# Optimization experiments

Hardware: AMD Instinct MI355X
Metric: run time of the kernel (lower is better)

The kernel has to match this reference:

```python
import jax, jax.numpy as jnp
import numpy as np

HEAD, DIM, R = 8, 256, 3
RA = (2 * R + 1) ** 2  # 49


def conv2d(x, w, b=None, pad=0, groups=1):
    y = jax.lax.conv_general_dilated(x, w, (1, 1), [(pad, pad), (pad, pad)],
                                     dimension_numbers=('NCHW', 'OIHW', 'NCHW'),
                                     feature_group_count=groups)
    return y if b is None else y + b[None, :, None, None]


def grid_sample(img, grid, mode, padding='zeros'):
    # img [B,C,H,W]; grid [B,Hg,Wg,2] with (x,y) in [-1,1]; align_corners=False.
    B, C, H, W = img.shape
    Hg, Wg = grid.shape[1], grid.shape[2]
    gx = ((grid[..., 0] + 1.0) * W - 1.0) / 2.0
    gy = ((grid[..., 1] + 1.0) * H - 1.0) / 2.0
    if padding == 'border':
        gx = jnp.clip(gx, 0.0, W - 1.0)
        gy = jnp.clip(gy, 0.0, H - 1.0)
    gx = gx.reshape(B, -1)
    gy = gy.reshape(B, -1)

    def gather(iy, ix):
        iyc = jnp.clip(iy, 0, H - 1)
        ixc = jnp.clip(ix, 0, W - 1)
        return jax.vmap(lambda im, a, b: im[:, a, b])(img, iyc, ixc)  # [B,C,N]

    def mask(iy, ix):
        if padding == 'border':
            return jnp.ones(iy.shape, img.dtype)
        return ((ix >= 0) & (ix < W) & (iy >= 0) & (iy < H)).astype(img.dtype)

    if mode == 'nearest':
        ix = jnp.round(gx).astype(jnp.int32)
        iy = jnp.round(gy).astype(jnp.int32)
        out = gather(iy, ix) * mask(iy, ix)[:, None, :]
    else:  # bilinear
        x0f = jnp.floor(gx); y0f = jnp.floor(gy)
        wx = gx - x0f; wy = gy - y0f
        x0 = x0f.astype(jnp.int32); y0 = y0f.astype(jnp.int32)
        out = jnp.zeros((B, C, gx.shape[1]), img.dtype)
        for dx, dy, w in ((0, 0, (1 - wx) * (1 - wy)), (1, 0, wx * (1 - wy)),
                          (0, 1, (1 - wx) * wy), (1, 1, wx * wy)):
            ix = x0 + dx; iy = y0 + dy
            out = out + gather(iy, ix) * (w * mask(iy, ix))[:, None, :]
    return out.reshape(B, C, Hg, Wg)


def mlp2(x, W1, b1, W2, b2):
    return jax.nn.relu(x @ W1.T + b1) @ W2.T + b2


def setup_inputs() -> dict:
    key = jax.random.key(0)
    ks = jax.random.split(key, 32)
    B, H, W, Q = 1, 64, 64, 4096
    f32 = jnp.float32
    rn = lambda k, shp, s=0.02: jax.random.normal(k, shp, f32) * s
    return {
        'inp': jax.random.normal(ks[0], (B, 3, H, W), f32),
        'coord': jax.random.uniform(ks[1], (B, Q, 2), f32, -1.0, 1.0),
        'cell': jnp.full((B, Q, 2), 2.0 / (2 * H), f32),
        'W_enc': rn(ks[2], (64, 3, 3, 3)), 'b_enc': jnp.zeros((64,), f32),
        'W_ch': rn(ks[3], (256, 64, 3, 3)), 'b_ch': jnp.zeros((256,), f32),
        'W_q': rn(ks[4], (256, 256, 3, 3)), 'b_q': jnp.zeros((256,), f32),
        'W_k': rn(ks[5], (256, 256, 3, 3)), 'b_k': jnp.zeros((256,), f32),
        'W_v': rn(ks[6], (256, 256, 3, 3)), 'b_v': jnp.zeros((256,), f32),
        'W_off1': rn(ks[7], (256, 32, 5, 5)), 'b_off1': jnp.zeros((256,), f32),
        'ln_g': jnp.ones((256,), f32), 'ln_b': jnp.zeros((256,), f32),
        'W_off2': rn(ks[8], (98, 256, 1, 1)),
        'Wc1': rn(ks[9], (256, 98)), 'bc1': jnp.zeros((256,), f32),
        'Wc2': rn(ks[10], (49, 256)), 'bc2': jnp.zeros((49,), f32),
        'Wi1': rn(ks[11], (256, 12546)), 'bi1': jnp.zeros((256,), f32),
        'Wi2': rn(ks[12], (3, 256)), 'bi2': jnp.zeros((3,), f32),
        'scale': 2,
    }


def reference(inp, coord, cell, W_enc, b_enc, W_ch, b_ch, W_q, b_q, W_k, b_k,
              W_v, b_v, W_off1, b_off1, ln_g, ln_b, W_off2, Wc1, bc1, Wc2, bc2,
              Wi1, bi1, Wi2, bi2, scale):
    B, _, H, W = inp.shape
    Q = coord.shape[1]
    # gen_feat: encoder stub (conv+relu) -> conv_ch -> q/k/v convs
    feat = conv2d(jax.nn.relu(conv2d(inp, W_enc, b_enc, pad=1)), W_ch, b_ch, pad=1)
    fq = conv2d(feat, W_q, b_q, pad=1)
    fk = conv2d(feat, W_k, b_k, pad=1)
    fv = conv2d(feat, W_v, b_v, pad=1)
    # offset branch: grouped 5x5 conv -> channelwise LN -> GELU -> 1x1 conv (no bias)
    o = conv2d(feat, W_off1, b_off1, pad=2, groups=8)
    oc = o.transpose(0, 2, 3, 1)
    mu = oc.mean(-1, keepdims=True)
    var = ((oc - mu) ** 2).mean(-1, keepdims=True)
    oc = (oc - mu) / jnp.sqrt(var + 1e-5) * ln_g + ln_b
    offsets = conv2d(jax.nn.gelu(oc.transpose(0, 3, 1, 2), approximate=False), W_off2, None, pad=0)  # [B,98,H,W]
    # LR coordinate grid (y,x) at pixel centers in [-1,1]
    ys = -1.0 + 1.0 / H + (2.0 / H) * jnp.arange(H, dtype=inp.dtype)
    xs = -1.0 + 1.0 / W + (2.0 / W) * jnp.arange(W, dtype=inp.dtype)
    coord_lr = jnp.broadcast_to(jnp.stack(jnp.meshgrid(ys, xs, indexing='ij'), 0)[None], (B, 2, H, W))
    sc = coord[:, :, None, :]          # [B,Q,1,2] (y,x)
    g = sc[..., ::-1]                  # (x,y) for grid_sample
    sck = grid_sample(coord_lr, g, 'nearest').transpose(0, 2, 3, 1)  # [B,Q,1,2]
    off = grid_sample(offsets, g, 'nearest').transpose(0, 2, 3, 1).reshape(B, Q, RA, 2)
    off = jnp.tanh(off) * jnp.array([1.0 / (H - 1.0), 1.0 / (W - 1.0)], inp.dtype) * 2.0
    d = jnp.linspace(-R, R, 2 * R + 1).astype(inp.dtype)
    delta = jnp.stack(jnp.meshgrid(d * (2.0 / H), d * (2.0 / W), indexing='ij'), -1).reshape(1, 1, RA, 2)
    sck = sck + delta + off            # [B,Q,49,2] sampling locs (y,x)
    q = grid_sample(fq, g, 'bilinear').transpose(0, 2, 3, 1).reshape(B, Q, HEAD, DIM // HEAD)
    k = grid_sample(fk, sck[..., ::-1], 'nearest').transpose(0, 2, 3, 1).reshape(B, Q, RA, HEAD, DIM // HEAD)
    v = grid_sample(fv, sck[..., ::-1], 'nearest').transpose(0, 2, 3, 1).reshape(B, Q, RA, HEAD, DIM // HEAD)
    attn_val = jnp.einsum('bqhd,bqkhd->bqkh', q, k) / np.sqrt(DIM // HEAD)  # [B,Q,49,8]
    rel = (sc - sck) * jnp.array([H, W], inp.dtype)  # [B,Q,49,2]
    wcoord = mlp2(rel.reshape(B * Q, RA * 2), Wc1, bc1, Wc2, bc2).reshape(B, Q, RA, 1)
    attn = jax.nn.softmax(wcoord + attn_val, axis=2)  # softmax over 49 samples
    feat_in = (v * attn[..., None]).reshape(B, Q, RA * DIM)
    rel_cell = cell * jnp.array([H, W], inp.dtype)
    feat_in = jnp.concatenate([feat_in, rel_cell], -1)  # [B,Q,12546]
    pred = mlp2(feat_in.reshape(B * Q, -1), Wi1, bi1, Wi2, bi2).reshape(B, Q, 3)
    skip = grid_sample(inp, g, 'bilinear', 'border')[:, :, :, 0].transpose(0, 2, 1)
    return pred + skip
```

## Files before the change

### kernel.cpp

```cpp
#include <hip/hip_runtime.h>
#include <hip/hip_bf16.h>


typedef unsigned short u16;
typedef unsigned int u32;
using frag_ab = __attribute__((ext_vector_type(8))) short;
using frag_cd = __attribute__((ext_vector_type(4))) float;

#define HW 4096
#define NQ 4096
#define KBIG 12576
#define SPLITK 16
#define KCHUNK 800
#define KQ 2304
#define QSPLIT 3
#define QCHUNK 768
#define NBLK_QKV (64 * 6 * QSPLIT)
#define NBLK_OFF1 (64 * 8)

static __device__ __forceinline__ u16 f2b(float f) {
  union { __hip_bfloat16 h; u16 u; } c; c.h = __float2bfloat16(f); return c.u;
}
static __device__ __forceinline__ float b2f(u16 v) {
  return __uint_as_float((u32)v << 16);
}
static __device__ __forceinline__ u32 pk2(float a, float b) {
  union { __hip_bfloat162 h; u32 u; } c;
  c.h = __float22bfloat162_rn(float2{a, b});
  return c.u;
}
static __device__ __forceinline__ void glds16(const u16* g, u16* l) {
  __builtin_amdgcn_global_load_lds(
      (const __attribute__((address_space(1))) u32*)(g),
      (__attribute__((address_space(3))) u32*)(l), 16, 0, 0);
}

#define BM 64
#define BN 64
#define BK 32
#define LDSS 40

__global__ __launch_bounds__(256)
void gemm_bt(const u16* __restrict__ A, const u16* __restrict__ Bt,
             void* __restrict__ Cv, const float* __restrict__ bias,
             int N, int K, int ldc, int flags,
             long sA, long sB, long sC, int sBias)
{
  __shared__ u16 As[BM * LDSS];
  __shared__ u16 Bs[BN * LDSS];
  const int z = blockIdx.z;
  A  += (long)z * sA;
  Bt += (long)z * sB;
  const float* bz = bias ? bias + (long)z * sBias : nullptr;

  const int tid  = threadIdx.x;
  const int m0   = blockIdx.x * BM;
  const int n0   = blockIdx.y * BN;
  const int wave = tid >> 6, lane = tid & 63;
  const int mw = (wave & 1) * 32, nw = (wave >> 1) * 32;
  const int lr = lane & 15, lk = lane >> 4;
  const int srow = tid >> 2, scol = (tid & 3) * 8;

  frag_cd acc[2][2] = {};
  const u16* aptr = A + (size_t)(m0 + srow) * K + scol;
  const bool bok  = (n0 + srow) < N;
  const u16* bptr = Bt + (size_t)(n0 + srow) * K + scol;

  uint4 av = *(const uint4*)(aptr);
  uint4 bv = bok ? *(const uint4*)(bptr) : uint4{0u, 0u, 0u, 0u};

  for (int k0 = 0; k0 < K; k0 += BK) {
    *(uint4*)&As[srow * LDSS + scol] = av;
    *(uint4*)&Bs[srow * LDSS + scol] = bv;
    __syncthreads();
    if (k0 + BK < K) {
      av = *(const uint4*)(aptr + k0 + BK);
      bv = bok ? *(const uint4*)(bptr + k0 + BK) : uint4{0u, 0u, 0u, 0u};
    }
    frag_ab af0 = *(const frag_ab*)&As[(mw      + lr) * LDSS + lk * 8];
    frag_ab af1 = *(const frag_ab*)&As[(mw + 16 + lr) * LDSS + lk * 8];
    frag_ab bf0 = *(const frag_ab*)&Bs[(nw      + lr) * LDSS + lk * 8];
    frag_ab bf1 = *(const frag_ab*)&Bs[(nw + 16 + lr) * LDSS + lk * 8];
    acc[0][0] = __builtin_amdgcn_mfma_f32_16x16x32_bf16(af0, bf0, acc[0][0], 0, 0, 0);
    acc[0][1] = __builtin_amdgcn_mfma_f32_16x16x32_bf16(af0, bf1, acc[0][1], 0, 0, 0);
    acc[1][0] = __builtin_amdgcn_mfma_f32_16x16x32_bf16(af1, bf0, acc[1][0], 0, 0, 0);
    acc[1][1] = __builtin_amdgcn_mfma_f32_16x16x32_bf16(af1, bf1, acc[1][1], 0, 0, 0);
    __syncthreads();
  }

  const bool relu = flags & 1;
  const bool obf  = flags & 2;
  #pragma unroll
  for (int i = 0; i < 2; i++)
    #pragma unroll
    for (int j = 0; j < 2; j++) {
      int col = n0 + nw + j * 16 + lr;
      if (col >= N) continue;
      float badd = bz ? bz[col] : 0.f;
      #pragma unroll
      for (int r = 0; r < 4; r++) {
        int row = m0 + mw + i * 16 + lk * 4 + r;
        float v = acc[i][j][r] + badd;
        if (relu) v = fmaxf(v, 0.f);
        size_t idx = (size_t)z * sC + (size_t)row * ldc + col;
        if (obf) ((u16*)Cv)[idx] = f2b(v);
        else     ((float*)Cv)[idx] = v;
      }
    }
}

template<int W3, int SH, int PAD>
__global__ __launch_bounds__(256)
void gemm_conv(const u16* __restrict__ feat, const u16* __restrict__ Bt,
               void* __restrict__ Cv, const float* __restrict__ bias,
               int N, int K, int ldc, int flags, int FC, int cbStride,
               long sB, long sC, int sBias)
{
  __shared__ u16 As[BM * LDSS];
  __shared__ u16 Bs[BN * LDSS];
  const int z = blockIdx.z;
  Bt += (long)z * sB;
  const float* bz = bias ? bias + (long)z * sBias : nullptr;
  const int cb = z * cbStride;

  const int tid  = threadIdx.x;
  const int m0   = blockIdx.x * BM;
  const int n0   = blockIdx.y * BN;
  const int wave = tid >> 6, lane = tid & 63;
  const int mw = (wave & 1) * 32, nw = (wave >> 1) * 32;
  const int lr = lane & 15, lk = lane >> 4;
  const int srow = tid >> 2, scol = (tid & 3) * 8;
  const int p = m0 + srow, y = p >> 6, x = p & 63;

  frag_cd acc[2][2] = {};
  const bool bok  = (n0 + srow) < N;
  const u16* bptr = Bt + (size_t)(n0 + srow) * K + scol;

  auto stageA = [&](int k0) -> uint4 {
    int k = k0 + scol;
    int s = k >> SH;
    int c = k & ((1 << SH) - 1);
    int dy = s / W3, dx = s - dy * W3;
    int yy = y + dy - PAD, xx = x + dx - PAD;
    if (((unsigned)yy < 64u) && ((unsigned)xx < 64u))
      return *(const uint4*)&feat[(size_t)(yy * 64 + xx) * FC + cb + c];
    return uint4{0u, 0u, 0u, 0u};
  };

  uint4 av = stageA(0);
  uint4 bv = bok ? *(const uint4*)(bptr) : uint4{0u, 0u, 0u, 0u};

  for (int k0 = 0; k0 < K; k0 += BK) {
    *(uint4*)&As[srow * LDSS + scol] = av;
    *(uint4*)&Bs[srow * LDSS + scol] = bv;
    __syncthreads();
    if (k0 + BK < K) {
      av = stageA(k0 + BK);
      bv = bok ? *(const uint4*)(bptr + k0 + BK) : uint4{0u, 0u, 0u, 0u};
    }
    frag_ab af0 = *(const frag_ab*)&As[(mw      + lr) * LDSS + lk * 8];
    frag_ab af1 = *(const frag_ab*)&As[(mw + 16 + lr) * LDSS + lk * 8];
    frag_ab bf0 = *(const frag_ab*)&Bs[(nw      + lr) * LDSS + lk * 8];
    frag_ab bf1 = *(const frag_ab*)&Bs[(nw + 16 + lr) * LDSS + lk * 8];
    acc[0][0] = __builtin_amdgcn_mfma_f32_16x16x32_bf16(af0, bf0, acc[0][0], 0, 0, 0);
    acc[0][1] = __builtin_amdgcn_mfma_f32_16x16x32_bf16(af0, bf1, acc[0][1], 0, 0, 0);
    acc[1][0] = __builtin_amdgcn_mfma_f32_16x16x32_bf16(af1, bf0, acc[1][0], 0, 0, 0);
    acc[1][1] = __builtin_amdgcn_mfma_f32_16x16x32_bf16(af1, bf1, acc[1][1], 0, 0, 0);
    __syncthreads();
  }

  const bool relu = flags & 1;
  const bool obf  = flags & 2;
  #pragma unroll
  for (int i = 0; i < 2; i++)
    #pragma unroll
    for (int j = 0; j < 2; j++) {
      int col = n0 + nw + j * 16 + lr;
      if (col >= N) continue;
      float badd = bz ? bz[col] : 0.f;
      #pragma unroll
      for (int r = 0; r < 4; r++) {
        int row = m0 + mw + i * 16 + lk * 4 + r;
        float v = acc[i][j][r] + badd;
        if (relu) v = fmaxf(v, 0.f);
        size_t idx = (size_t)z * sC + (size_t)row * ldc + col;
        if (obf) ((u16*)Cv)[idx] = f2b(v);
        else     ((float*)Cv)[idx] = v;
      }
    }
}

__global__ __launch_bounds__(256)
void gemm_feat(const u16* __restrict__ feat, const u16* __restrict__ Btqkv,
               u16* __restrict__ Pq, const u16* __restrict__ Btoff1,
               float* __restrict__ obuf, const float* __restrict__ b_off1)
{
  __shared__ u16 smem[6656];
  const int bid = blockIdx.x;
  const int tid = threadIdx.x;
  const int wave = tid >> 6, lane = tid & 63;
  const int lr = lane & 15, lk = lane >> 4;

  if (bid < NBLK_QKV) {
    u16* As = smem;
    u16* Bs = smem + 64 * 40;
    const int mz  = bid & 63;
    const int rest = bid >> 6;
    const int ny  = rest % 6;
    const int z   = rest / 6;
    const int m0  = mz * 64;
    const int n0  = ny * 128;
    const int kbeg = z * QCHUNK;
    const int kend = kbeg + QCHUNK;
    const int nw = wave * 32;
    const int arow = tid >> 2, acol = (tid & 3) * 8;
    const int p = m0 + arow, y = p >> 6, x = p & 63;

    frag_cd acc[4][2] = {};
    const u16* bbase = Btqkv + (size_t)(n0 + (tid >> 2)) * KQ + (tid & 3) * 8 + kbeg;
    u16* bdst = &Bs[(size_t)tid * 8];

    auto stageA = [&](int k0) -> uint4 {
      int k = k0 + acol;
      int s = k >> 8, c = k & 255;
      int dy = s / 3, dx = s - dy * 3;
      int yy = y + dy - 1, xx = x + dx - 1;
      if (((unsigned)yy < 64u) && ((unsigned)xx < 64u))
        return *(const uint4*)&feat[(size_t)(yy * 64 + xx) * 256 + c];
      return uint4{0u, 0u, 0u, 0u};
    };

    uint4 av = stageA(kbeg);

    for (int k0 = kbeg; k0 < kend; k0 += BK) {
      glds16(bbase + (k0 - kbeg), bdst);
      glds16(bbase + (k0 - kbeg) + (size_t)64 * KQ, bdst + 2048);
      *(uint4*)&As[arow * LDSS + acol] = av;
      __syncthreads();
      if (k0 + BK < kend) av = stageA(k0 + BK);
      frag_ab af[4];
      #pragma unroll
      for (int i = 0; i < 4; i++)
        af[i] = *(const frag_ab*)&As[(i * 16 + lr) * LDSS + lk * 8];
      #pragma unroll
      for (int j = 0; j < 2; j++) {
        frag_ab bf = *(const frag_ab*)&Bs[(nw + j * 16 + lr) * 32 + lk * 8];
        #pragma unroll
        for (int i = 0; i < 4; i++)
          acc[i][j] = __builtin_amdgcn_mfma_f32_16x16x32_bf16(af[i], bf, acc[i][j], 0, 0, 0);
      }
      __syncthreads();
    }

    #pragma unroll
    for (int i = 0; i < 4; i++)
      #pragma unroll
      for (int j = 0; j < 2; j++) {
        int col = n0 + nw + j * 16 + lr;
        #pragma unroll
        for (int r = 0; r < 4; r++) {
          int row = m0 + i * 16 + lk * 4 + r;
          Pq[(size_t)z * (NQ * 768) + (size_t)row * 768 + col] = f2b(acc[i][j][r]);
        }
      }
  } else {
    u16* As = smem;
    u16* Bs = smem + 64 * 40;
    const int t  = bid - NBLK_QKV;
    const int m0 = (t & 63) * 64;
    const int g  = t >> 6;
    const int cb = g * 32;
    const u16* Bt = Btoff1 + (size_t)g * 32 * 800;
    const float* bz = b_off1 + g * 32;
    const int mw = (wave & 1) * 32, nw = (wave >> 1) * 32;
    const int srow = tid >> 2, scol = (tid & 3) * 8;
    const int p = m0 + srow, y = p >> 6, x = p & 63;

    frag_cd acc[2][2] = {};
    const bool bok  = srow < 32;
    const u16* bptr = Bt + (size_t)srow * 800 + scol;

    auto stageA = [&](int k0) -> uint4 {
      int k = k0 + scol;
      int s = k >> 5;
      int c = k & 31;
      int dy = s / 5, dx = s - dy * 5;
      int yy = y + dy - 2, xx = x + dx - 2;
      if (((unsigned)yy < 64u) && ((unsigned)xx < 64u))
        return *(const uint4*)&feat[(size_t)(yy * 64 + xx) * 256 + cb + c];
      return uint4{0u, 0u, 0u, 0u};
    };

    uint4 av = stageA(0);
    uint4 bv = bok ? *(const uint4*)(bptr) : uint4{0u, 0u, 0u, 0u};

    for (int k0 = 0; k0 < 800; k0 += BK) {
      *(uint4*)&As[srow * LDSS + scol] = av;
      *(uint4*)&Bs[srow * LDSS + scol] = bv;
      __syncthreads();
      if (k0 + BK < 800) {
        av = stageA(k0 + BK);
        bv = bok ? *(const uint4*)(bptr + k0 + BK) : uint4{0u, 0u, 0u, 0u};
      }
      frag_ab af0 = *(const frag_ab*)&As[(mw      + lr) * LDSS + lk * 8];
      frag_ab af1 = *(const frag_ab*)&As[(mw + 16 + lr) * LDSS + lk * 8];
      frag_ab bf0 = *(const frag_ab*)&Bs[(nw      + lr) * LDSS + lk * 8];
      frag_ab bf1 = *(const frag_ab*)&Bs[(nw + 16 + lr) * LDSS + lk * 8];
      acc[0][0] = __builtin_amdgcn_mfma_f32_16x16x32_bf16(af0, bf0, acc[0][0], 0, 0, 0);
      acc[0][1] = __builtin_amdgcn_mfma_f32_16x16x32_bf16(af0, bf1, acc[0][1], 0, 0, 0);
      acc[1][0] = __builtin_amdgcn_mfma_f32_16x16x32_bf16(af1, bf0, acc[1][0], 0, 0, 0);
      acc[1][1] = __builtin_amdgcn_mfma_f32_16x16x32_bf16(af1, bf1, acc[1][1], 0, 0, 0);
      __syncthreads();
    }

    #pragma unroll
    for (int i = 0; i < 2; i++)
      #pragma unroll
      for (int j = 0; j < 2; j++) {
        int col = nw + j * 16 + lr;
        if (col >= 32) continue;
        float badd = bz[col];
        #pragma unroll
        for (int r = 0; r < 4; r++) {
          int row = m0 + mw + i * 16 + lk * 4 + r;
          obuf[(size_t)row * 256 + g * 32 + col] = acc[i][j][r] + badd;
        }
      }
  }
}

__global__ __launch_bounds__(256)
void reduce_qkv(const u16* __restrict__ P, const float* __restrict__ bias,
                u16* __restrict__ outb, float* __restrict__ outV)
{
  int i8 = blockIdx.x * 256 + threadIdx.x;
  if (i8 >= NQ * 96) return;
  size_t i = (size_t)i8 * 8;
  int row = (int)(i / 768);
  int c = (int)(i % 768);
  float v[8];
  #pragma unroll
  for (int t = 0; t < 8; t++) v[t] = bias[c + t];
  for (int z = 0; z < QSPLIT; z++) {
    uint4 a = *(const uint4*)&P[(size_t)z * (NQ * 768) + i];
    u32 aw[4] = {a.x, a.y, a.z, a.w};
    #pragma unroll
    for (int t = 0; t < 4; t++) {
      v[2 * t]     += __uint_as_float(aw[t] << 16);
      v[2 * t + 1] += __uint_as_float(aw[t] & 0xffff0000u);
    }
  }
  uint4 ob = {pk2(v[0], v[1]), pk2(v[2], v[3]), pk2(v[4], v[5]), pk2(v[6], v[7])};
  *(uint4*)&outb[i] = ob;
  if (c >= 512) {
    float* dst = outV + (size_t)row * 256 + (c - 512);
    *(float4*)dst       = float4{v[0], v[1], v[2], v[3]};
    *(float4*)(dst + 4) = float4{v[4], v[5], v[6], v[7]};
  }
}

__global__ __launch_bounds__(512, 4)
void gemm_big(const u16* __restrict__ Bt, const float* __restrict__ fqkvV,
              const float* __restrict__ attnval, const int* __restrict__ vidx,
              const float* __restrict__ cell, u16* __restrict__ P)
{
  __shared__ u16 As[128 * LDSS];
  __shared__ u16 Bs[256 * 32];
  __shared__ int   s_vidx[5 * 128];
  __shared__ float s_attn[5 * 128 * 8];
  const int tid  = threadIdx.x;
  const int m0   = blockIdx.x * 128;
  const int z    = blockIdx.y;
  const int kbeg = z * KCHUNK;
  const int kend = min(KBIG, kbeg + KCHUNK);
  const int jbeg = kbeg >> 8;
  const int jcnt = ((kend - 1) >> 8) - jbeg + 1;
  const int wave = tid >> 6, lane = tid & 63;
  const int mw = (wave & 1) * 64, nwv = (wave >> 1) * 64;
  const int lr = lane & 15, lk = lane >> 4;
  const int arow = tid >> 2, acol = (tid & 3) * 8;
  const int q = m0 + arow;

  for (int t = tid; t < 128 * jcnt; t += 512) {
    int r = t & 127, jj = t >> 7;
    int j = jbeg + jj;
    s_vidx[t] = (j < 49) ? vidx[(m0 + r) * 49 + j] : -1;
  }
  for (int t = tid; t < 128 * 8 * jcnt; t += 512) {
    int h = t & 7, rr = (t >> 3) & 127, jj = t >> 10;
    int j = jbeg + jj;
    s_attn[t] = (j < 49) ? attnval[((size_t)((m0 + rr) * 49 + j)) * 8 + h] : 0.f;
  }
  __syncthreads();

  auto loadA = [&](int k0, float4& f0, float4& f1, float& w) {
    const int k = k0 + acol;
    const int j = k >> 8, c = k & 255;
    f0 = float4{0.f, 0.f, 0.f, 0.f};
    f1 = float4{0.f, 0.f, 0.f, 0.f};
    w = 0.f;
    if (j < 49) {
      const int jj = j - jbeg;
      int id = s_vidx[jj * 128 + arow];
      if (id >= 0) {
        w = s_attn[(jj * 128 + arow) * 8 + (c >> 5)];
        const float* src = fqkvV + (size_t)id * 256 + c;
        f0 = *(const float4*)src;
        f1 = *(const float4*)(src + 4);
      }
    } else if (c == 0) {
      f0.x = cell[q * 2]; f0.y = cell[q * 2 + 1];
      w = 64.f;
    }
  };

  frag_cd acc[4][4] = {};
  float4 f0c, f1c; float wc_;
  loadA(kbeg, f0c, f1c, wc_);
  const u16* bbase = Bt + (size_t)(tid >> 2) * KBIG + (tid & 3) * 8 + kbeg;
  u16* bdst = &Bs[(size_t)tid * 8];

  for (int k0 = kbeg; k0 < kend; k0 += BK) {
    glds16(bbase + (k0 - kbeg), bdst);
    glds16(bbase + (k0 - kbeg) + (size_t)128 * KBIG, bdst + 4096);
    {
      uint4 av;
      av.x = pk2(f0c.x * wc_, f0c.y * wc_);
      av.y = pk2(f0c.z * wc_, f0c.w * wc_);
      av.z = pk2(f1c.x * wc_, f1c.y * wc_);
      av.w = pk2(f1c.z * wc_, f1c.w * wc_);
      *(uint4*)&As[arow * LDSS + acol] = av;
    }
    __syncthreads();
    if (k0 + BK < kend) loadA(k0 + BK, f0c, f1c, wc_);
    frag_ab af[4];
    #pragma unroll
    for (int i = 0; i < 4; i++)
      af[i] = *(const frag_ab*)&As[(mw + i * 16 + lr) * LDSS + lk * 8];
    #pragma unroll
    for (int j = 0; j < 4; j++) {
      frag_ab bf = *(const frag_ab*)&Bs[(nwv + j * 16 + lr) * 32 + lk * 8];
      #pragma unroll
      for (int i = 0; i < 4; i++)
        acc[i][j] = __builtin_amdgcn_mfma_f32_16x16x32_bf16(af[i], bf, acc[i][j], 0, 0, 0);
    }
    __syncthreads();
  }

  #pragma unroll
  for (int i = 0; i < 4; i++)
    #pragma unroll
    for (int j = 0; j < 4; j++) {
      int col = nwv + j * 16 + lr;
      #pragma unroll
      for (int r = 0; r < 4; r++) {
        int row = m0 + mw + i * 16 + lk * 4 + r;
        P[(size_t)z * (NQ * 256) + (size_t)row * 256 + col] = f2b(acc[i][j][r]);
      }
    }
}

__global__ __launch_bounds__(256)
void reduce_final(const u16* __restrict__ Pb, const float* __restrict__ bi1,
                  const float* __restrict__ Wi2, const float* __restrict__ bi2,
                  const float* __restrict__ skipb, float* __restrict__ out)
{
  const int q = blockIdx.x, c = threadIdx.x;
  float s = 0.f;
  #pragma unroll
  for (int z = 0; z < SPLITK; z++)
    s += b2f(Pb[(size_t)z * (NQ * 256) + (size_t)q * 256 + c]);
  s += bi1[c];
  s = fmaxf(s, 0.f);

  __shared__ float part[3][4];
  float p0 = s * Wi2[c], p1 = s * Wi2[256 + c], p2 = s * Wi2[512 + c];
  #pragma unroll
  for (int off = 32; off; off >>= 1) {
    p0 += __shfl_xor(p0, off);
    p1 += __shfl_xor(p1, off);
    p2 += __shfl_xor(p2, off);
  }
  if ((c & 63) == 0) {
    int w = c >> 6;
    part[0][w] = p0; part[1][w] = p1; part[2][w] = p2;
  }
  __syncthreads();
  if (c < 3)
    out[q * 3 + c] = bi2[c] + skipb[q * 3 + c]
                   + part[c][0] + part[c][1] + part[c][2] + part[c][3];
}

__global__ __launch_bounds__(512)
void softmax_k(const float* __restrict__ wc, float* __restrict__ attnval)
{
  const int q = blockIdx.x;
  const int tid = threadIdx.x;
  const int hh = tid >> 6, l = tid & 63;
  float v = (l < 49) ? wc[(size_t)q * 49 + l] + attnval[((size_t)q * 49 + l) * 8 + hh]
                     : -1e30f;
  float m = v;
  #pragma unroll
  for (int off = 32; off; off >>= 1) m = fmaxf(m, __shfl_xor(m, off));
  float e = (l < 49) ? expf(v - m) : 0.f;
  float s = e;
  #pragma unroll
  for (int off = 32; off; off >>= 1) s += __shfl_xor(s, off);
  if (l < 49) attnval[((size_t)q * 49 + l) * 8 + hh] = e / s;
}

static __device__ __forceinline__
void packconv(const float* __restrict__ W, u16* __restrict__ Bt,
              int Cin, int K2, int idx)
{
  int o  = idx / (Cin * K2);
  int r  = idx - o * (Cin * K2);
  int ci = r / K2;
  int s  = r - ci * K2;
  Bt[(size_t)o * (Cin * K2) + s * Cin + ci] = f2b(W[idx]);
}
static __device__ __forceinline__
void packcast(const float* __restrict__ W, u16* __restrict__ Bt,
              int Kin, int Kout, int idx)
{
  int n = idx / Kout, k = idx - n * Kout;
  Bt[idx] = f2b(k < Kin ? W[(size_t)n * Kin + k] : 0.f);
}

#define SZ_CH   147456
#define SZ_QKV  589824
#define SZ_OFF1 204800
#define SZ_OFF2 25088
#define SZ_C1   32768
#define SZ_C2   12544
#define SZ_WI1  3219456
#define SZ_PACK (SZ_CH + 3*SZ_QKV + SZ_OFF1 + SZ_OFF2 + SZ_C1 + SZ_C2 + 768 + SZ_WI1)

__global__ void pack_all(const float* W_ch, const float* W_q, const float* W_k,
                         const float* W_v, const float* W_off1, const float* W_off2,
                         const float* Wc1, const float* Wc2, const float* Wi1,
                         const float* b_q, const float* b_k, const float* b_v,
                         u16* Btch, u16* Btqkv, u16* Btoff1, u16* Btoff2,
                         u16* Btc1, u16* Btc2, u16* Wi1p, float* bqkv)
{
  int i = blockIdx.x * 256 + threadIdx.x;
  if (i < SZ_CH) { packconv(W_ch, Btch, 64, 9, i); return; }
  i -= SZ_CH;
  if (i < SZ_QKV) { packconv(W_q, Btqkv, 256, 9, i); return; }
  i -= SZ_QKV;
  if (i < SZ_QKV) { packconv(W_k, Btqkv + (size_t)256 * 2304, 256, 9, i); return; }
  i -= SZ_QKV;
  if (i < SZ_QKV) { packconv(W_v, Btqkv + (size_t)512 * 2304, 256, 9, i); return; }
  i -= SZ_QKV;
  if (i < SZ_OFF1) { packconv(W_off1, Btoff1, 32, 25, i); return; }
  i -= SZ_OFF1;
  if (i < SZ_OFF2) { packcast(W_off2, Btoff2, 256, 256, i); return; }
  i -= SZ_OFF2;
  if (i < SZ_C1) { packcast(Wc1, Btc1, 98, 128, i); return; }
  i -= SZ_C1;
  if (i < SZ_C2) { packcast(Wc2, Btc2, 256, 256, i); return; }
  i -= SZ_C2;
  if (i < 768) {
    bqkv[i] = (i < 256) ? b_q[i] : (i < 512) ? b_k[i - 256] : b_v[i - 512];
    return;
  }
  i -= 768;
  if (i < SZ_WI1) { packcast(Wi1, Wi1p, 12546, 12576, i); }
}

__global__ __launch_bounds__(64)
void conv_enc(const float* __restrict__ inp, const float* __restrict__ W,
              const float* __restrict__ b, u16* __restrict__ feat1)
{
  const int p = blockIdx.x, c = threadIdx.x;
  const int y = p >> 6, x = p & 63;
  float s = b[c];
  #pragma unroll
  for (int ci = 0; ci < 3; ci++)
    #pragma unroll
    for (int dy = 0; dy < 3; dy++) {
      int yy = y + dy - 1;
      if ((unsigned)yy >= 64u) continue;
      #pragma unroll
      for (int dx = 0; dx < 3; dx++) {
        int xx = x + dx - 1;
        if ((unsigned)xx >= 64u) continue;
        s += inp[ci * HW + yy * 64 + xx] * W[((c * 3 + ci) * 3 + dy) * 3 + dx];
      }
    }
  feat1[(size_t)p * 64 + c] = f2b(fmaxf(s, 0.f));
}

__global__ __launch_bounds__(256)
void ln_gelu(const float* __restrict__ x, const float* __restrict__ g,
             const float* __restrict__ b, u16* __restrict__ y)
{
  const int p = blockIdx.x, c = threadIdx.x;
  __shared__ float r1[4], r2[4];
  float v = x[(size_t)p * 256 + c];
  float s1 = v, s2 = v * v;
  #pragma unroll
  for (int off = 32; off; off >>= 1) {
    s1 += __shfl_xor(s1, off);
    s2 += __shfl_xor(s2, off);
  }
  if ((c & 63) == 0) { r1[c >> 6] = s1; r2[c >> 6] = s2; }
  __syncthreads();
  float t1 = r1[0] + r1[1] + r1[2] + r1[3];
  float t2 = r2[0] + r2[1] + r2[2] + r2[3];
  float mu  = t1 * (1.f / 256.f);
  float var = t2 * (1.f / 256.f) - mu * mu;
  float xn = (v - mu) * rsqrtf(var + 1e-5f) * g[c] + b[c];
  float ge = 0.5f * xn * (1.f + erff(xn * 0.70710678118654752f));
  y[(size_t)p * 256 + c] = f2b(ge);
}

__global__ __launch_bounds__(256)
void sampler(const float* __restrict__ coord, const u16* __restrict__ fqkvb,
             const float* __restrict__ offs, const float* __restrict__ inp,
             float* __restrict__ attnval, u16* __restrict__ relbuf,
             int* __restrict__ vidx, float* __restrict__ skipb)
{
  const int q = blockIdx.x;
  const int tid = threadIdx.x;
  __shared__ float s_off[98];
  __shared__ int s_idx[49];
  __shared__ float s_q[256];

  const float c0 = coord[q * 2], c1 = coord[q * 2 + 1];
  const float gxp = ((c1 + 1.f) * 64.f - 1.f) * 0.5f;
  const float gyp = ((c0 + 1.f) * 64.f - 1.f) * 0.5f;
  const int ixn = (int)rintf(gxp), iyn = (int)rintf(gyp);
  const bool inn = ((unsigned)ixn < 64u) && ((unsigned)iyn < 64u);

  if (tid < 98) {
    float v = inn ? offs[(size_t)(iyn * 64 + ixn) * 98 + tid] : 0.f;
    s_off[tid] = tanhf(v) * (2.f / 63.f);
  }
  __syncthreads();

  const float scky = inn ? (-1.f + (float)(2 * iyn + 1) * (1.f / 64.f)) : 0.f;
  const float sckx = inn ? (-1.f + (float)(2 * ixn + 1) * (1.f / 64.f)) : 0.f;

  if (tid < 49) {
    const int a = tid / 7, bb = tid - a * 7;
    float sy = scky + (float)(a - 3) * (2.f / 64.f) + s_off[2 * tid];
    float sx = sckx + (float)(bb - 3) * (2.f / 64.f) + s_off[2 * tid + 1];
    relbuf[(size_t)q * 128 + 2 * tid]     = f2b((c0 - sy) * 64.f);
    relbuf[(size_t)q * 128 + 2 * tid + 1] = f2b((c1 - sx) * 64.f);
    float gx2 = ((sx + 1.f) * 64.f - 1.f) * 0.5f;
    float gy2 = ((sy + 1.f) * 64.f - 1.f) * 0.5f;
    int ix2 = (int)rintf(gx2), iy2 = (int)rintf(gy2);
    int id = (((unsigned)ix2 < 64u) && ((unsigned)iy2 < 64u)) ? (iy2 * 64 + ix2) : -1;
    s_idx[tid] = id;
    vidx[q * 49 + tid] = id;
  } else if (tid >= 98 && tid < 128) {
    relbuf[(size_t)q * 128 + tid] = 0;
  }

  {
    const float x0f = floorf(gxp), y0f = floorf(gyp);
    const float wx = gxp - x0f, wy = gyp - y0f;
    const int x0 = (int)x0f, y0 = (int)y0f;
    float qc = 0.f;
    #pragma unroll
    for (int t = 0; t < 4; t++) {
      int xi = x0 + (t & 1), yi = y0 + (t >> 1);
      if (((unsigned)xi < 64u) && ((unsigned)yi < 64u)) {
        float w = ((t & 1) ? wx : 1.f - wx) * ((t >> 1) ? wy : 1.f - wy);
        qc += w * b2f(fqkvb[(size_t)(yi * 64 + xi) * 768 + tid]);
      }
    }
    s_q[tid] = qc * 0.17677669529663687f;
  }

  if (tid < 3) {
    float gx = fminf(fmaxf(gxp, 0.f), 63.f);
    float gy = fminf(fmaxf(gyp, 0.f), 63.f);
    float xf = floorf(gx), yf = floorf(gy);
    float wxs = gx - xf, wys = gy - yf;
    int xa = (int)xf, ya = (int)yf;
    int xb = min(xa + 1, 63), yb = min(ya + 1, 63);
    const float* ch = inp + tid * HW;
    float v = (1.f - wxs) * (1.f - wys) * ch[ya * 64 + xa]
            + wxs * (1.f - wys) * ch[ya * 64 + xb]
            + (1.f - wxs) * wys * ch[yb * 64 + xa]
            + wxs * wys * ch[yb * 64 + xb];
    skipb[q * 3 + tid] = v;
  }
  __syncthreads();

  const int wave = tid >> 6, lane = tid & 63;
  const int half = lane >> 5, sub = lane & 31;
  const int ch0 = sub * 8;
  const int h = sub >> 2;
  float qv[8];
  #pragma unroll
  for (int i = 0; i < 8; i++) qv[i] = s_q[ch0 + i];

  for (int it = 0; it < 7; it++) {
    int j = it * 8 + wave * 2 + half;
    if (j >= 49) break;
    int id = s_idx[j];
    float p = 0.f;
    if (id >= 0) {
      uint4 kv = *(const uint4*)&fqkvb[(size_t)id * 768 + 256 + ch0];
      u32 w0 = kv.x, w1 = kv.y, w2 = kv.z, w3 = kv.w;
      p = fmaf(qv[0], __uint_as_float(w0 << 16), p);
      p = fmaf(qv[1], __uint_as_float(w0 & 0xffff0000u), p);
      p = fmaf(qv[2], __uint_as_float(w1 << 16), p);
      p = fmaf(qv[3], __uint_as_float(w1 & 0xffff0000u), p);
      p = fmaf(qv[4], __uint_as_float(w2 << 16), p);
      p = fmaf(qv[5], __uint_as_float(w2 & 0xffff0000u), p);
      p = fmaf(qv[6], __uint_as_float(w3 << 16), p);
      p = fmaf(qv[7], __uint_as_float(w3 & 0xffff0000u), p);
    }
    p += __shfl_down(p, 2, 4);
    p += __shfl_down(p, 1, 4);
    if ((sub & 3) == 0) attnval[((size_t)q * 49 + j) * 8 + h] = p;
  }
}

extern "C" void kernel_launch(void* const* d_in, const int* in_sizes, int n_in,
                              void* d_out, int out_size, void* d_ws, size_t ws_size,
                              hipStream_t stream)
{
  const float* inp    = (const float*)d_in[0];
  const float* coord  = (const float*)d_in[1];
  const float* cell   = (const float*)d_in[2];
  const float* W_enc  = (const float*)d_in[3];
  const float* b_enc  = (const float*)d_in[4];
  const float* W_ch   = (const float*)d_in[5];
  const float* b_ch   = (const float*)d_in[6];
  const float* W_q    = (const float*)d_in[7];
  const float* b_q    = (const float*)d_in[8];
  const float* W_k    = (const float*)d_in[9];
  const float* b_k    = (const float*)d_in[10];
  const float* W_v    = (const float*)d_in[11];
  const float* b_v    = (const float*)d_in[12];
  const float* W_off1 = (const float*)d_in[13];
  const float* b_off1 = (const float*)d_in[14];
  const float* ln_g   = (const float*)d_in[15];
  const float* ln_b   = (const float*)d_in[16];
  const float* W_off2 = (const float*)d_in[17];
  const float* Wc1    = (const float*)d_in[18];
  const float* bc1    = (const float*)d_in[19];
  const float* Wc2    = (const float*)d_in[20];
  const float* bc2    = (const float*)d_in[21];
  const float* Wi1    = (const float*)d_in[22];
  const float* bi1    = (const float*)d_in[23];
  const float* Wi2    = (const float*)d_in[24];
  const float* bi2    = (const float*)d_in[25];

  char* base = (char*)d_ws;
  size_t off = 0;
  auto alloc = [&](size_t bytes) -> char* {
    char* r = base + off;
    off = (off + bytes + 255) & ~(size_t)255;
    return r;
  };

  float* obuf   = (float*)alloc((size_t)HW * 256 * 4);
  u16*   ocg    = (u16*)  alloc((size_t)HW * 256 * 2);
  float* offsb  = (float*)alloc((size_t)HW * 98 * 4);
  u16*   feat1  = (u16*)  alloc((size_t)HW * 64 * 2);
  u16*   feat   = (u16*)  alloc((size_t)HW * 256 * 2);
  u16*   hid1   = (u16*)  alloc((size_t)NQ * 256 * 2);
  float* wcb    = (float*)alloc((size_t)NQ * 49 * 4);
  u16*   relbuf = (u16*)  alloc((size_t)NQ * 128 * 2);
  u16*   Btqkv  = (u16*)  alloc((size_t)768 * 2304 * 2);
  u16*   Btch   = (u16*)  alloc((size_t)256 * 576 * 2);
  u16*   Btoff1 = (u16*)  alloc((size_t)256 * 800 * 2);
  u16*   Btoff2 = (u16*)  alloc((size_t)98 * 256 * 2);
  u16*   Btc1   = (u16*)  alloc((size_t)256 * 128 * 2);
  u16*   Btc2   = (u16*)  alloc((size_t)49 * 256 * 2);
  u16* Pb = (u16*)base;
  u16* Pqb = (u16*)(base + ((size_t)36 << 20));
  {
    size_t need = ((size_t)36 << 20) + (size_t)QSPLIT * NQ * 768 * 2;
    if (off < need) off = (need + 255) & ~(size_t)255;
  }
  u16*   fqkvb   = (u16*)  alloc((size_t)HW * 768 * 2);
  float* fqkvV   = (float*)alloc((size_t)HW * 256 * 4);
  float* attnval = (float*)alloc((size_t)NQ * 49 * 8 * 4);
  int*   vidxb   = (int*)  alloc((size_t)NQ * 49 * 4);
  float* skipb   = (float*)alloc((size_t)NQ * 3 * 4);
  u16*   Wi1p    = (u16*)  alloc((size_t)256 * KBIG * 2);
  float* bqkv    = (float*)alloc(768 * 4);
  (void)ws_size; (void)in_sizes; (void)n_in; (void)out_size;

  pack_all<<<(SZ_PACK + 255) / 256, 256, 0, stream>>>(
      W_ch, W_q, W_k, W_v, W_off1, W_off2, Wc1, Wc2, Wi1, b_q, b_k, b_v,
      Btch, Btqkv, Btoff1, Btoff2, Btc1, Btc2, Wi1p, bqkv);

  conv_enc<<<HW, 64, 0, stream>>>(inp, W_enc, b_enc, feat1);
  gemm_conv<3, 6, 1><<<dim3(64, 4, 1), 256, 0, stream>>>(
      feat1, Btch, feat, b_ch, 256, 576, 256, 2, 64, 0, 0, 0, 0);
  gemm_feat<<<NBLK_QKV + NBLK_OFF1, 256, 0, stream>>>(
      feat, Btqkv, Pqb, Btoff1, obuf, b_off1);
  reduce_qkv<<<(NQ * 96 + 255) / 256, 256, 0, stream>>>(Pqb, bqkv, fqkvb, fqkvV);
  ln_gelu<<<HW, 256, 0, stream>>>(obuf, ln_g, ln_b, ocg);
  gemm_bt<<<dim3(64, 2, 1), 256, 0, stream>>>(ocg, Btoff2, offsb, nullptr,
      98, 256, 98, 0, 0, 0, 0, 0);

  sampler<<<NQ, 256, 0, stream>>>(coord, fqkvb, offsb, inp,
                                  attnval, relbuf, vidxb, skipb);
  gemm_bt<<<dim3(64, 4, 1), 256, 0, stream>>>(relbuf, Btc1, hid1, bc1,
      256, 128, 256, 3, 0, 0, 0, 0);
  gemm_bt<<<dim3(64, 1, 1), 256, 0, stream>>>(hid1, Btc2, wcb, bc2,
      49, 256, 49, 0, 0, 0, 0, 0);
  softmax_k<<<NQ, 512, 0, stream>>>(wcb, attnval);

  gemm_big<<<dim3(32, SPLITK), 512, 0, stream>>>(
      Wi1p, fqkvV, attnval, vidxb, cell, Pb);
  reduce_final<<<NQ, 256, 0, stream>>>(Pb, bi1, Wi2, bi2, skipb, (float*)d_out);
}
```

Baseline: 287.8 us.

## Merge small kernels to cut launch count and fold Wc2 GEMM into softmax

Three independent kernels are merged into the blocks of neighbouring launches: the encoder conv now runs as extra blocks of the weight-pack kernel, and the LayerNorm+GELU blocks share a launch with the QKV split-K reduction. The small 49-wide Wc2 GEMM is removed and computed per query inside the softmax kernel in fp32 against a transposed, padded copy of Wc2, which also drops the wcb intermediate buffer. The goal is fewer launches and less tail idle time between tiny kernels. The cost is that the second coord-MLP layer now runs as scalar FMAs instead of matrix cores, with extra shared-memory reductions in every softmax block.

```diff
diff --git a/kernel.cpp b/kernel.cpp
--- a/kernel.cpp
+++ b/kernel.cpp
@@ -17,6 +17,7 @@
 #define QCHUNK 768
 #define NBLK_QKV (64 * 6 * QSPLIT)
 #define NBLK_OFF1 (64 * 8)
+#define NBLK_RQ (NQ * 96 / 256)
 
 static __device__ __forceinline__ u16 f2b(float f) {
   union { __hip_bfloat16 h; u16 u; } c; c.h = __float2bfloat16(f); return c.u;
@@ -330,32 +331,57 @@
 }
 
 __global__ __launch_bounds__(256)
-void reduce_qkv(const u16* __restrict__ P, const float* __restrict__ bias,
-                u16* __restrict__ outb, float* __restrict__ outV)
-{
-  int i8 = blockIdx.x * 256 + threadIdx.x;
-  if (i8 >= NQ * 96) return;
-  size_t i = (size_t)i8 * 8;
-  int row = (int)(i / 768);
-  int c = (int)(i % 768);
-  float v[8];
-  #pragma unroll
-  for (int t = 0; t < 8; t++) v[t] = bias[c + t];
-  for (int z = 0; z < QSPLIT; z++) {
-    uint4 a = *(const uint4*)&P[(size_t)z * (NQ * 768) + i];
-    u32 aw[4] = {a.x, a.y, a.z, a.w};
-    #pragma unroll
-    for (int t = 0; t < 4; t++) {
-      v[2 * t]     += __uint_as_float(aw[t] << 16);
-      v[2 * t + 1] += __uint_as_float(aw[t] & 0xffff0000u);
-    }
-  }
-  uint4 ob = {pk2(v[0], v[1]), pk2(v[2], v[3]), pk2(v[4], v[5]), pk2(v[6], v[7])};
-  *(uint4*)&outb[i] = ob;
-  if (c >= 512) {
-    float* dst = outV + (size_t)row * 256 + (c - 512);
-    *(float4*)dst       = float4{v[0], v[1], v[2], v[3]};
-    *(float4*)(dst + 4) = float4{v[4], v[5], v[6], v[7]};
+void mid_fuse(const u16* __restrict__ P, const float* __restrict__ bias,
+              u16* __restrict__ outb, float* __restrict__ outV,
+              const float* __restrict__ xo, const float* __restrict__ g,
+              const float* __restrict__ bl, u16* __restrict__ y)
+{
+  __shared__ float r1[4], r2[4];
+  const int bid = blockIdx.x;
+  const int tid = threadIdx.x;
+
+  if (bid < NBLK_RQ) {
+    int i8 = bid * 256 + tid;
+    size_t i = (size_t)i8 * 8;
+    int row = (int)(i / 768);
+    int c = (int)(i % 768);
+    float v[8];
+    #pragma unroll
+    for (int t = 0; t < 8; t++) v[t] = bias[c + t];
+    for (int z = 0; z < QSPLIT; z++) {
+      uint4 a = *(const uint4*)&P[(size_t)z * (NQ * 768) + i];
+      u32 aw[4] = {a.x, a.y, a.z, a.w};
+      #pragma unroll
+      for (int t = 0; t < 4; t++) {
+        v[2 * t]     += __uint_as_float(aw[t] << 16);
+        v[2 * t + 1] += __uint_as_float(aw[t] & 0xffff0000u);
+      }
+    }
+    uint4 ob = {pk2(v[0], v[1]), pk2(v[2], v[3]), pk2(v[4], v[5]), pk2(v[6], v[7])};
+    *(uint4*)&outb[i] = ob;
+    if (c >= 512) {
+      float* dst = outV + (size_t)row * 256 + (c - 512);
+      *(float4*)dst       = float4{v[0], v[1], v[2], v[3]};
+      *(float4*)(dst + 4) = float4{v[4], v[5], v[6], v[7]};
+    }
+  } else {
+    const int p = bid - NBLK_RQ, c = tid;
+    float v = xo[(size_t)p * 256 + c];
+    float s1 = v, s2 = v * v;
+    #pragma unroll
+    for (int off = 32; off; off >>= 1) {
+      s1 += __shfl_xor(s1, off);
+      s2 += __shfl_xor(s2, off);
+    }
+    if ((c & 63) == 0) { r1[c >> 6] = s1; r2[c >> 6] = s2; }
+    __syncthreads();
+    float t1 = r1[0] + r1[1] + r1[2] + r1[3];
+    float t2 = r2[0] + r2[1] + r2[2] + r2[3];
+    float mu  = t1 * (1.f / 256.f);
+    float var = t2 * (1.f / 256.f) - mu * mu;
+    float xn = (v - mu) * rsqrtf(var + 1e-5f) * g[c] + bl[c];
+    float ge = 0.5f * xn * (1.f + erff(xn * 0.70710678118654752f));
+    y[(size_t)p * 256 + c] = f2b(ge);
   }
 }
 
@@ -492,13 +518,35 @@
 }
 
 __global__ __launch_bounds__(512)
-void softmax_k(const float* __restrict__ wc, float* __restrict__ attnval)
-{
+void softmax_wc(const u16* __restrict__ hid1, const float* __restrict__ Wc2t,
+                const float* __restrict__ bc2, float* __restrict__ attnval)
+{
+  __shared__ float s_h[256];
+  __shared__ float s_part[8][64];
+  __shared__ float s_wc[64];
   const int q = blockIdx.x;
   const int tid = threadIdx.x;
-  const int hh = tid >> 6, l = tid & 63;
-  float v = (l < 49) ? wc[(size_t)q * 49 + l] + attnval[((size_t)q * 49 + l) * 8 + hh]
-                     : -1e30f;
+  const int wave = tid >> 6, l = tid & 63;
+
+  if (tid < 256) s_h[tid] = b2f(hid1[(size_t)q * 256 + tid]);
+  __syncthreads();
+
+  float p = 0.f;
+  const float* wcol = Wc2t + (size_t)(wave * 32) * 64 + l;
+  const float* h = s_h + wave * 32;
+  #pragma unroll
+  for (int k = 0; k < 32; k++) p = fmaf(h[k], wcol[(size_t)k * 64], p);
+  s_part[wave][l] = p;
+  __syncthreads();
+  if (tid < 64) {
+    float s = s_part[0][tid] + s_part[1][tid] + s_part[2][tid] + s_part[3][tid]
+            + s_part[4][tid] + s_part[5][tid] + s_part[6][tid] + s_part[7][tid];
+    s_wc[tid] = s + ((tid < 49) ? bc2[tid] : 0.f);
+  }
+  __syncthreads();
+
+  const int hh = wave;
+  float v = (l < 49) ? s_wc[l] + attnval[((size_t)q * 49 + l) * 8 + hh] : -1e30f;
   float m = v;
   #pragma unroll
   for (int off = 32; off; off >>= 1) m = fmaxf(m, __shfl_xor(m, off));
@@ -532,17 +580,42 @@
 #define SZ_OFF1 204800
 #define SZ_OFF2 25088
 #define SZ_C1   32768
-#define SZ_C2   12544
+#define SZ_C2T  16384
 #define SZ_WI1  3219456
-#define SZ_PACK (SZ_CH + 3*SZ_QKV + SZ_OFF1 + SZ_OFF2 + SZ_C1 + SZ_C2 + 768 + SZ_WI1)
-
-__global__ void pack_all(const float* W_ch, const float* W_q, const float* W_k,
-                         const float* W_v, const float* W_off1, const float* W_off2,
-                         const float* Wc1, const float* Wc2, const float* Wi1,
-                         const float* b_q, const float* b_k, const float* b_v,
-                         u16* Btch, u16* Btqkv, u16* Btoff1, u16* Btoff2,
-                         u16* Btc1, u16* Btc2, u16* Wi1p, float* bqkv)
-{
+#define SZ_PACK (SZ_CH + 3*SZ_QKV + SZ_OFF1 + SZ_OFF2 + SZ_C1 + SZ_C2T + 768 + SZ_WI1)
+#define PACKBLK ((SZ_PACK + 255) / 256)
+#define CONVBLK 1024
+
+__global__ void pack_conv(const float* W_ch, const float* W_q, const float* W_k,
+                          const float* W_v, const float* W_off1, const float* W_off2,
+                          const float* Wc1, const float* Wc2, const float* Wi1,
+                          const float* b_q, const float* b_k, const float* b_v,
+                          u16* Btch, u16* Btqkv, u16* Btoff1, u16* Btoff2,
+                          u16* Btc1, float* Wc2t, u16* Wi1p, float* bqkv,
+                          const float* inp, const float* W_enc,
+                          const float* b_enc, u16* feat1)
+{
+  if (blockIdx.x >= PACKBLK) {
+    int t = (blockIdx.x - PACKBLK) * 256 + threadIdx.x;
+    int p = t >> 6, c = t & 63;
+    const int y = p >> 6, x = p & 63;
+    float s = b_enc[c];
+    #pragma unroll
+    for (int ci = 0; ci < 3; ci++)
+      #pragma unroll
+      for (int dy = 0; dy < 3; dy++) {
+        int yy = y + dy - 1;
+        if ((unsigned)yy >= 64u) continue;
+        #pragma unroll
+        for (int dx = 0; dx < 3; dx++) {
+          int xx = x + dx - 1;
+          if ((unsigned)xx >= 64u) continue;
+          s += inp[ci * HW + yy * 64 + xx] * W_enc[((c * 3 + ci) * 3 + dy) * 3 + dx];
+        }
+      }
+    feat1[(size_t)p * 64 + c] = f2b(fmaxf(s, 0.f));
+    return;
+  }
   int i = blockIdx.x * 256 + threadIdx.x;
   if (i < SZ_CH) { packconv(W_ch, Btch, 64, 9, i); return; }
   i -= SZ_CH;
@@ -558,61 +631,18 @@
   i -= SZ_OFF2;
   if (i < SZ_C1) { packcast(Wc1, Btc1, 98, 128, i); return; }
   i -= SZ_C1;
-  if (i < SZ_C2) { packcast(Wc2, Btc2, 256, 256, i); return; }
-  i -= SZ_C2;
+  if (i < SZ_C2T) {
+    int k = i >> 6, l = i & 63;
+    Wc2t[i] = (l < 49) ? Wc2[(size_t)l * 256 + k] : 0.f;
+    return;
+  }
+  i -= SZ_C2T;
   if (i < 768) {
     bqkv[i] = (i < 256) ? b_q[i] : (i < 512) ? b_k[i - 256] : b_v[i - 512];
     return;
   }
   i -= 768;
   if (i < SZ_WI1) { packcast(Wi1, Wi1p, 12546, 12576, i); }
-}
-
-__global__ __launch_bounds__(64)
-void conv_enc(const float* __restrict__ inp, const float* __restrict__ W,
-              const float* __restrict__ b, u16* __restrict__ feat1)
-{
-  const int p = blockIdx.x, c = threadIdx.x;
-  const int y = p >> 6, x = p & 63;
-  float s = b[c];
-  #pragma unroll
-  for (int ci = 0; ci < 3; ci++)
-    #pragma unroll
-    for (int dy = 0; dy < 3; dy++) {
-      int yy = y + dy - 1;
-      if ((unsigned)yy >= 64u) continue;
-      #pragma unroll
-      for (int dx = 0; dx < 3; dx++) {
-        int xx = x + dx - 1;
-        if ((unsigned)xx >= 64u) continue;
-        s += inp[ci * HW + yy * 64 + xx] * W[((c * 3 + ci) * 3 + dy) * 3 + dx];
-      }
-    }
-  feat1[(size_t)p * 64 + c] = f2b(fmaxf(s, 0.f));
-}
-
-__global__ __launch_bounds__(256)
-void ln_gelu(const float* __restrict__ x, const float* __restrict__ g,
-             const float* __restrict__ b, u16* __restrict__ y)
-{
-  const int p = blockIdx.x, c = threadIdx.x;
-  __shared__ float r1[4], r2[4];
-  float v = x[(size_t)p * 256 + c];
-  float s1 = v, s2 = v * v;
-  #pragma unroll
-  for (int off = 32; off; off >>= 1) {
-    s1 += __shfl_xor(s1, off);
-    s2 += __shfl_xor(s2, off);
-  }
-  if ((c & 63) == 0) { r1[c >> 6] = s1; r2[c >> 6] = s2; }
-  __syncthreads();
-  float t1 = r1[0] + r1[1] + r1[2] + r1[3];
-  float t2 = r2[0] + r2[1] + r2[2] + r2[3];
-  float mu  = t1 * (1.f / 256.f);
-  float var = t2 * (1.f / 256.f) - mu * mu;
-  float xn = (v - mu) * rsqrtf(var + 1e-5f) * g[c] + b[c];
-  float ge = 0.5f * xn * (1.f + erff(xn * 0.70710678118654752f));
-  y[(size_t)p * 256 + c] = f2b(ge);
 }
 
 __global__ __launch_bounds__(256)
@@ -766,14 +796,13 @@
   u16*   feat1  = (u16*)  alloc((size_t)HW * 64 * 2);
   u16*   feat   = (u16*)  alloc((size_t)HW * 256 * 2);
   u16*   hid1   = (u16*)  alloc((size_t)NQ * 256 * 2);
-  float* wcb    = (float*)alloc((size_t)NQ * 49 * 4);
   u16*   relbuf = (u16*)  alloc((size_t)NQ * 128 * 2);
   u16*   Btqkv  = (u16*)  alloc((size_t)768 * 2304 * 2);
   u16*   Btch   = (u16*)  alloc((size_t)256 * 576 * 2);
   u16*   Btoff1 = (u16*)  alloc((size_t)256 * 800 * 2);
   u16*   Btoff2 = (u16*)  alloc((size_t)98 * 256 * 2);
   u16*   Btc1   = (u16*)  alloc((size_t)256 * 128 * 2);
-  u16*   Btc2   = (u16*)  alloc((size_t)49 * 256 * 2);
+  float* Wc2t   = (float*)alloc((size_t)256 * 64 * 4);
   u16* Pb = (u16*)base;
   u16* Pqb = (u16*)(base + ((size_t)36 << 20));
   {
@@ -789,17 +818,17 @@
   float* bqkv    = (float*)alloc(768 * 4);
   (void)ws_size; (void)in_sizes; (void)n_in; (void)out_size;
 
-  pack_all<<<(SZ_PACK + 255) / 256, 256, 0, stream>>>(
+  pack_conv<<<PACKBLK + CONVBLK, 256, 0, stream>>>(
       W_ch, W_q, W_k, W_v, W_off1, W_off2, Wc1, Wc2, Wi1, b_q, b_k, b_v,
-      Btch, Btqkv, Btoff1, Btoff2, Btc1, Btc2, Wi1p, bqkv);
-
-  conv_enc<<<HW, 64, 0, stream>>>(inp, W_enc, b_enc, feat1);
+      Btch, Btqkv, Btoff1, Btoff2, Btc1, Wc2t, Wi1p, bqkv,
+      inp, W_enc, b_enc, feat1);
+
   gemm_conv<3, 6, 1><<<dim3(64, 4, 1), 256, 0, stream>>>(
       feat1, Btch, feat, b_ch, 256, 576, 256, 2, 64, 0, 0, 0, 0);
   gemm_feat<<<NBLK_QKV + NBLK_OFF1, 256, 0, stream>>>(
       feat, Btqkv, Pqb, Btoff1, obuf, b_off1);
-  reduce_qkv<<<(NQ * 96 + 255) / 256, 256, 0, stream>>>(Pqb, bqkv, fqkvb, fqkvV);
-  ln_gelu<<<HW, 256, 0, stream>>>(obuf, ln_g, ln_b, ocg);
+  mid_fuse<<<NBLK_RQ + HW, 256, 0, stream>>>(
+      Pqb, bqkv, fqkvb, fqkvV, obuf, ln_g, ln_b, ocg);
   gemm_bt<<<dim3(64, 2, 1), 256, 0, stream>>>(ocg, Btoff2, offsb, nullptr,
       98, 256, 98, 0, 0, 0, 0, 0);
 
@@ -807,9 +836,7 @@
                                   attnval, relbuf, vidxb, skipb);
   gemm_bt<<<dim3(64, 4, 1), 256, 0, stream>>>(relbuf, Btc1, hid1, bc1,
       256, 128, 256, 3, 0, 0, 0, 0);
-  gemm_bt<<<dim3(64, 1, 1), 256, 0, stream>>>(hid1, Btc2, wcb, bc2,
-      49, 256, 49, 0, 0, 0, 0, 0);
-  softmax_k<<<NQ, 512, 0, stream>>>(wcb, attnval);
+  softmax_wc<<<NQ, 512, 0, stream>>>(hid1, Wc2t, bc2, attnval);
 
   gemm_big<<<dim3(32, SPLITK), 512, 0, stream>>>(
       Wi1p, fqkvV, attnval, vidxb, cell, Pb);
```

Result: no change. 288.0 us (+0.1%).
